# Kernel optimization log

Measured on AMD Instinct MI355X. Metric: run time of the kernel, lower is better.

## Reference

```python
import jax, jax.numpy as jnp
import numpy as np

N = 100000
E = 3200000
IN_DIM = 128
HD = 64
HEADS = 4
NEG_SLOPE = 0.2


def setup_inputs() -> dict:
    key = jax.random.key(0)
    ks = jax.random.split(key, 12)
    s = lambda fan_in: 1.0 / np.sqrt(fan_in)
    x = jax.random.normal(ks[0], (N, IN_DIM), dtype=jnp.float32)
    edge_index = jax.random.randint(ks[1], (2, E), 0, N, dtype=jnp.int64)
    W1 = jax.random.normal(ks[2], (IN_DIM, HEADS * HD), dtype=jnp.float32) * s(IN_DIM)
    a_src1 = jax.random.normal(ks[3], (HEADS, HD), dtype=jnp.float32) * s(HD)
    a_dst1 = jax.random.normal(ks[4], (HEADS, HD), dtype=jnp.float32) * s(HD)
    b1 = jnp.zeros((HEADS * HD,), dtype=jnp.float32)
    W2 = jax.random.normal(ks[5], (HEADS * HD, HD), dtype=jnp.float32) * s(HEADS * HD)
    a_src2 = jax.random.normal(ks[6], (1, HD), dtype=jnp.float32) * s(HD)
    a_dst2 = jax.random.normal(ks[7], (1, HD), dtype=jnp.float32) * s(HD)
    b2 = jnp.zeros((HD,), dtype=jnp.float32)
    lin_w = jax.random.normal(ks[8], (HD, 2), dtype=jnp.float32) * s(HD)
    lin_b = jnp.zeros((2,), dtype=jnp.float32)
    return {"x": x, "edge_index": edge_index, "W1": W1, "a_src1": a_src1,
            "a_dst1": a_dst1, "b1": b1, "W2": W2, "a_src2": a_src2,
            "a_dst2": a_dst2, "b2": b2, "lin_w": lin_w, "lin_b": lin_b}


def gat_conv(x, src, dst, W, a_src, a_dst, bias, heads, out_dim, concat):
    n = x.shape[0]
    h = (x @ W).reshape(n, heads, out_dim)                 # [N,H,D]
    alpha_s = jnp.einsum('nhd,hd->nh', h, a_src)           # [N,H]
    alpha_d = jnp.einsum('nhd,hd->nh', h, a_dst)           # [N,H]
    e = alpha_s[src] + alpha_d[dst]                        # [Etot,H]
    e = jnp.where(e > 0, e, NEG_SLOPE * e)                 # leaky relu
    m = jax.ops.segment_max(e, dst, num_segments=n)        # scatter-softmax (stable)
    m = jnp.where(jnp.isfinite(m), m, 0.0)
    e = jnp.exp(e - m[dst])
    denom = jax.ops.segment_sum(e, dst, num_segments=n)
    alpha = e / denom[dst]                                 # [Etot,H]
    out = jax.ops.segment_sum(h[src] * alpha[:, :, None], dst, num_segments=n)  # [N,H,D]
    out = out.reshape(n, heads * out_dim) if concat else out.mean(axis=1)
    return out + bias


def reference(x, edge_index, W1, a_src1, a_dst1, b1, W2, a_src2, a_dst2, b2, lin_w, lin_b):
    n = x.shape[0]
    loops = jnp.arange(n, dtype=edge_index.dtype)
    src = jnp.concatenate([edge_index[0], loops])          # add self-loops (PyG default)
    dst = jnp.concatenate([edge_index[1], loops])
    h = gat_conv(x, src, dst, W1, a_src1, a_dst1, b1, HEADS, HD, True)
    h = jax.nn.elu(h)
    h = gat_conv(h, src, dst, W2, a_src2, a_dst2, b2, 1, HD, True)
    h = jax.nn.elu(h)
    return h @ lin_w + lin_b                               # [N,2]
```

## Files before the change

### kernel.cpp

```cpp
#include <hip/hip_runtime.h>
#include <hip/hip_fp16.h>
#include <math.h>

#define NN 100000
#define EE 3200000
#define ETOT (EE + NN)
#define NEG_SLOPE 0.2f
#define DMAX 96
#define CHUNK 4096
#define NB0 ((ETOT + CHUNK - 1) / CHUNK)
#define RB 391
#define CAP 16384

typedef _Float16 half8 __attribute__((ext_vector_type(8)));
typedef _Float16 half4v __attribute__((ext_vector_type(4)));
typedef float floatx4 __attribute__((ext_vector_type(4)));

__device__ __forceinline__ float wsum64(float v) {
#pragma unroll
  for (int o = 32; o; o >>= 1) v += __shfl_xor(v, o);
  return v;
}
__device__ __forceinline__ float lrelu(float v) { return v > 0.f ? v : NEG_SLOPE * v; }
__device__ __forceinline__ float elu1(float v) { return v > 0.f ? v : expm1f(v); }

__global__ void k_init(int* __restrict__ ccur) {
  ccur[threadIdx.x] = threadIdx.x * CAP;
}

__global__ __launch_bounds__(256) void k_pass1(const int* __restrict__ ei,
                                               int* __restrict__ ccur,
                                               unsigned* __restrict__ ebuf,
                                               const float* __restrict__ W1,
                                               const float* __restrict__ W2,
                                               _Float16* __restrict__ W1t,
                                               _Float16* __restrict__ W2t) {
  int b = blockIdx.x;
  if (b >= NB0) {
    int idx = (b - NB0) * 256 + threadIdx.x;
    if (idx < 32768) {
      int n = idx >> 7, k = idx & 127;
      W1t[idx] = (_Float16)W1[k * 256 + n];
    } else {
      int j = idx - 32768;
      int n = j >> 8, k = j & 255;
      W2t[j] = (_Float16)W2[k * 64 + n];
    }
    return;
  }
  __shared__ unsigned vv[CHUNK];
  __shared__ unsigned short cbv[CHUNK];
  __shared__ int h[256];
  __shared__ int cur[256];
  int t = threadIdx.x;
  h[t] = 0;
  __syncthreads();
  int base = b * CHUNK;
  int lim = base + CHUNK; if (lim > ETOT) lim = ETOT;
  int cnt = lim - base;
  for (int i = t; i < cnt; i += 256) {
    int e = base + i;
    int s, d;
    if (e < EE) { s = ei[e]; d = ei[EE + e]; } else { s = e - EE; d = s; }
    unsigned cb = (unsigned)d / (unsigned)RB;
    unsigned dloc = (unsigned)d - cb * (unsigned)RB;
    vv[i] = (dloc << 17) | (unsigned)s;
    cbv[i] = (unsigned short)cb;
    atomicAdd(&h[cb], 1);
  }
  __syncthreads();
  if (h[t]) cur[t] = atomicAdd(&ccur[t], h[t]);
  __syncthreads();
  for (int i = t; i < cnt; i += 256) {
    int cb = cbv[i];
    int pos = atomicAdd(&cur[cb], 1);
    ebuf[pos] = vv[i];
  }
}

__global__ __launch_bounds__(256) void k_pass2(const unsigned* __restrict__ ebuf,
                                               const int* __restrict__ ccur,
                                               int* __restrict__ offs,
                                               int* __restrict__ degarr,
                                               int* __restrict__ csr) {
  __shared__ unsigned ed[CAP];
  __shared__ int hist[RB];
  __shared__ int cur[RB];
  int b = blockIdx.x, t = threadIdx.x;
  int d0 = b * RB;
  int rb = NN - d0; if (rb > RB) rb = RB;
  int w0 = b * CAP;
  int cnt = ccur[b] - w0;
  if (cnt > CAP) cnt = CAP;
  for (int j = t; j < rb; j += 256) hist[j] = 0;
  __syncthreads();
  for (int i = t; i < cnt; i += 256) {
    unsigned v = ebuf[w0 + i];
    ed[i] = v;
    atomicAdd(&hist[v >> 17], 1);
  }
  __syncthreads();
  if (t == 0) {
    int run = w0;
    for (int j = 0; j < rb; ++j) { cur[j] = run; run += hist[j]; }
  }
  __syncthreads();
  for (int j = t; j < rb; j += 256) {
    offs[d0 + j] = cur[j];
    degarr[d0 + j] = hist[j];
  }
  __syncthreads();
  for (int i = t; i < cnt; i += 256) {
    unsigned v = ed[i];
    int pos = atomicAdd(&cur[v >> 17], 1);
    csr[pos] = (int)(v & 0x1FFFFu);
  }
}

__global__ __launch_bounds__(256) void k_gemm1m(const float* __restrict__ x,
                                                const _Float16* __restrict__ W1t,
                                                const float* __restrict__ a_src,
                                                const float* __restrict__ a_dst,
                                                _Float16* __restrict__ h1h,
                                                float* __restrict__ as_out,
                                                float* __restrict__ ad_out) {
  __shared__ _Float16 As[64][136];
  __shared__ _Float16 Wt[128][136];
  const int bx = blockIdx.x & 1;
  const int by = blockIdx.x >> 1;
  const int tid = threadIdx.x;
  const int row0 = by * 64;
#pragma unroll
  for (int i = 0; i < 8; ++i) {
    int idx = i * 256 + tid;
    int r = idx >> 5;
    int c4 = (idx & 31) * 4;
    int gr = row0 + r;
    float4 f = make_float4(0.f, 0.f, 0.f, 0.f);
    if (gr < NN) f = *(const float4*)(x + (size_t)gr * 128 + c4);
    half4v h; h[0] = (_Float16)f.x; h[1] = (_Float16)f.y; h[2] = (_Float16)f.z; h[3] = (_Float16)f.w;
    *(half4v*)&As[r][c4] = h;
  }
#pragma unroll
  for (int i = 0; i < 8; ++i) {
    int idx = i * 256 + tid;
    int r = idx >> 4;
    int g = idx & 15;
    *(half8*)&Wt[r][g * 8] = *(const half8*)(W1t + (size_t)(bx * 128 + r) * 128 + g * 8);
  }
  __syncthreads();

  const int wid = tid >> 6, lane = tid & 63;
  const int m16 = lane & 15, quad = lane >> 4;
  floatx4 acc[8];
#pragma unroll
  for (int nt = 0; nt < 8; ++nt) acc[nt] = (floatx4){0.f, 0.f, 0.f, 0.f};
#pragma unroll
  for (int ks = 0; ks < 4; ++ks) {
    half8 av = *(half8*)&As[wid * 16 + m16][ks * 32 + quad * 8];
#pragma unroll
    for (int nt = 0; nt < 8; ++nt) {
      half8 bv = *(half8*)&Wt[nt * 16 + m16][ks * 32 + quad * 8];
      acc[nt] = __builtin_amdgcn_mfma_f32_16x16x32_f16(av, bv, acc[nt], 0, 0, 0);
    }
  }
  float asr[8], adr[8];
#pragma unroll
  for (int nt = 0; nt < 8; ++nt) {
    asr[nt] = a_src[bx * 128 + nt * 16 + m16];
    adr[nt] = a_dst[bx * 128 + nt * 16 + m16];
  }
#pragma unroll
  for (int r = 0; r < 4; ++r) {
    int gr = row0 + wid * 16 + quad * 4 + r;
    bool ok = gr < NN;
#pragma unroll
    for (int hp = 0; hp < 2; ++hp) {
      float ps = 0.f, pd = 0.f;
#pragma unroll
      for (int j = 0; j < 4; ++j) {
        ps = fmaf(acc[hp * 4 + j][r], asr[hp * 4 + j], ps);
        pd = fmaf(acc[hp * 4 + j][r], adr[hp * 4 + j], pd);
      }
#pragma unroll
      for (int o = 1; o < 16; o <<= 1) { ps += __shfl_xor(ps, o); pd += __shfl_xor(pd, o); }
      if (ok && m16 == 0) {
        as_out[gr * 4 + bx * 2 + hp] = ps;
        ad_out[gr * 4 + bx * 2 + hp] = pd;
      }
    }
    if (ok) {
#pragma unroll
      for (int nt = 0; nt < 8; ++nt)
        h1h[(size_t)gr * 256 + bx * 128 + nt * 16 + m16] = (_Float16)acc[nt][r];
    }
  }
}

__global__ __launch_bounds__(256) void k_gemm2m(const _Float16* __restrict__ h1e,
                                                const _Float16* __restrict__ W2t,
                                                const float* __restrict__ a_src,
                                                const float* __restrict__ a_dst,
                                                _Float16* __restrict__ h2h,
                                                float* __restrict__ as_out,
                                                float* __restrict__ ad_out) {
  __shared__ _Float16 As2[64][136];
  __shared__ _Float16 Wt2[64][264];
  const int by = blockIdx.x;
  const int tid = threadIdx.x;
  const int row0 = by * 64;
#pragma unroll
  for (int i = 0; i < 8; ++i) {
    int idx = i * 256 + tid;
    int r = idx >> 5;
    int g = idx & 31;
    *(half8*)&Wt2[r][g * 8] = *(const half8*)(W2t + (size_t)r * 256 + g * 8);
  }
  const int wid = tid >> 6, lane = tid & 63;
  const int m16 = lane & 15, quad = lane >> 4;
  floatx4 acc[4];
#pragma unroll
  for (int nt = 0; nt < 4; ++nt) acc[nt] = (floatx4){0.f, 0.f, 0.f, 0.f};

  for (int kc = 0; kc < 2; ++kc) {
#pragma unroll
    for (int i = 0; i < 4; ++i) {
      int idx = i * 256 + tid;
      int r = idx >> 4;
      int g = idx & 15;
      int gr = row0 + r;
      half8 v = {0, 0, 0, 0, 0, 0, 0, 0};
      if (gr < NN) v = *(const half8*)(h1e + (size_t)gr * 256 + kc * 128 + g * 8);
      *(half8*)&As2[r][g * 8] = v;
    }
    __syncthreads();
#pragma unroll
    for (int ks = 0; ks < 4; ++ks) {
      half8 av = *(half8*)&As2[wid * 16 + m16][ks * 32 + quad * 8];
#pragma unroll
      for (int nt = 0; nt < 4; ++nt) {
        half8 bv = *(half8*)&Wt2[nt * 16 + m16][kc * 128 + ks * 32 + quad * 8];
        acc[nt] = __builtin_amdgcn_mfma_f32_16x16x32_f16(av, bv, acc[nt], 0, 0, 0);
      }
    }
    __syncthreads();
  }
  float asr[4], adr[4];
#pragma unroll
  for (int nt = 0; nt < 4; ++nt) {
    asr[nt] = a_src[nt * 16 + m16];
    adr[nt] = a_dst[nt * 16 + m16];
  }
#pragma unroll
  for (int r = 0; r < 4; ++r) {
    float ps = 0.f, pd = 0.f;
#pragma unroll
    for (int nt = 0; nt < 4; ++nt) {
      ps = fmaf(acc[nt][r], asr[nt], ps);
      pd = fmaf(acc[nt][r], adr[nt], pd);
    }
#pragma unroll
    for (int o = 1; o < 16; o <<= 1) { ps += __shfl_xor(ps, o); pd += __shfl_xor(pd, o); }
    int gr = row0 + wid * 16 + quad * 4 + r;
    if (gr < NN) {
      if (m16 == 0) { as_out[gr] = ps; ad_out[gr] = pd; }
#pragma unroll
      for (int nt = 0; nt < 4; ++nt)
        h2h[(size_t)gr * 64 + nt * 16 + m16] = (_Float16)acc[nt][r];
    }
  }
}

__global__ __launch_bounds__(256) void k_attn1(const int* __restrict__ offs,
                                               const int* __restrict__ degarr,
                                               const int* __restrict__ csr_src,
                                               const float* __restrict__ a_s,
                                               const float* __restrict__ a_d,
                                               const _Float16* __restrict__ h1h,
                                               const float* __restrict__ b1,
                                               _Float16* __restrict__ h1e) {
  __shared__ float alpha[4][DMAX][4];
  __shared__ int sidx[4][DMAX];
  const int wid = threadIdx.x >> 6;
  const int n = blockIdx.x * 4 + wid;
  const int lane = threadIdx.x & 63;
  const int beg = offs[n], deg = degarr[n];
  const float4 ad = *(const float4*)(a_d + n * 4);
  float4 sm = make_float4(0.f, 0.f, 0.f, 0.f);
  for (int d = lane; d < deg; d += 64) {
    int s = csr_src[beg + d];
    float4 as = *(const float4*)(a_s + s * 4);
    float e0 = __expf(lrelu(as.x + ad.x));
    float e1 = __expf(lrelu(as.y + ad.y));
    float e2 = __expf(lrelu(as.z + ad.z));
    float e3 = __expf(lrelu(as.w + ad.w));
    sm.x += e0; sm.y += e1; sm.z += e2; sm.w += e3;
    if (d < DMAX) {
      sidx[wid][d] = s;
      *(float4*)&alpha[wid][d][0] = make_float4(e0, e1, e2, e3);
    }
  }
  sm.x = wsum64(sm.x); sm.y = wsum64(sm.y); sm.z = wsum64(sm.z); sm.w = wsum64(sm.w);
  const float4 inv4 = make_float4(1.f / sm.x, 1.f / sm.y, 1.f / sm.z, 1.f / sm.w);
  const int dlim = deg < DMAX ? deg : DMAX;
  for (int d = lane; d < dlim; d += 64) {
    float4 a = *(float4*)&alpha[wid][d][0];
    a.x *= inv4.x; a.y *= inv4.y; a.z *= inv4.z; a.w *= inv4.w;
    *(float4*)&alpha[wid][d][0] = a;
  }
  const int half = lane >> 5;
  const int sub = lane & 31;
  const int head = sub >> 3;
  const _Float16* __restrict__ hb = h1h + sub * 8;
  float accv[8];
#pragma unroll
  for (int j = 0; j < 8; ++j) accv[j] = 0.f;
  int d = 0;
  for (; d + 8 <= dlim; d += 8) {
    int ss[4]; float ww[4];
#pragma unroll
    for (int u = 0; u < 4; ++u) {
      int idx = d + 2 * u + half;
      ss[u] = sidx[wid][idx];
      ww[u] = alpha[wid][idx][head];
    }
    half8 rr[4];
#pragma unroll
    for (int u = 0; u < 4; ++u)
      rr[u] = *(const half8*)(hb + (size_t)ss[u] * 256);
#pragma unroll
    for (int u = 0; u < 4; ++u) {
#pragma unroll
      for (int j = 0; j < 8; ++j)
        accv[j] = fmaf((float)rr[u][j], ww[u], accv[j]);
    }
  }
  for (; d + 2 <= dlim; d += 2) {
    int idx = d + half;
    int s = sidx[wid][idx];
    float w = alpha[wid][idx][head];
    half8 r = *(const half8*)(hb + (size_t)s * 256);
#pragma unroll
    for (int j = 0; j < 8; ++j) accv[j] = fmaf((float)r[j], w, accv[j]);
  }
  if (d < dlim) {
    int s = sidx[wid][d];
    float w = half ? 0.f : alpha[wid][d][head];
    half8 r = *(const half8*)(hb + (size_t)s * 256);
#pragma unroll
    for (int j = 0; j < 8; ++j) accv[j] = fmaf((float)r[j], w, accv[j]);
  }
  if (deg > DMAX) {
    const float adh = head == 0 ? ad.x : head == 1 ? ad.y : head == 2 ? ad.z : ad.w;
    const float invh = head == 0 ? inv4.x : head == 1 ? inv4.y : head == 2 ? inv4.z : inv4.w;
    if (!half) {
      for (int dd = DMAX; dd < deg; ++dd) {
        int s = csr_src[beg + dd];
        float w = __expf(lrelu(a_s[s * 4 + head] + adh)) * invh;
        half8 r = *(const half8*)(hb + (size_t)s * 256);
#pragma unroll
        for (int j = 0; j < 8; ++j) accv[j] = fmaf((float)r[j], w, accv[j]);
      }
    }
  }
#pragma unroll
  for (int j = 0; j < 8; ++j) accv[j] += __shfl_xor(accv[j], 32);
  if (!half) {
    const int c = sub * 8;
    float4 b0 = *(const float4*)(b1 + c);
    float4 b1v = *(const float4*)(b1 + c + 4);
    half8 o;
    o[0] = (_Float16)elu1(accv[0] + b0.x);
    o[1] = (_Float16)elu1(accv[1] + b0.y);
    o[2] = (_Float16)elu1(accv[2] + b0.z);
    o[3] = (_Float16)elu1(accv[3] + b0.w);
    o[4] = (_Float16)elu1(accv[4] + b1v.x);
    o[5] = (_Float16)elu1(accv[5] + b1v.y);
    o[6] = (_Float16)elu1(accv[6] + b1v.z);
    o[7] = (_Float16)elu1(accv[7] + b1v.w);
    *(half8*)(h1e + (size_t)n * 256 + c) = o;
  }
}

__global__ __launch_bounds__(256) void k_attn2(const int* __restrict__ offs,
                                               const int* __restrict__ degarr,
                                               const int* __restrict__ csr_src,
                                               const float* __restrict__ a_s,
                                               const float* __restrict__ a_d,
                                               const _Float16* __restrict__ h2h,
                                               const float* __restrict__ b2,
                                               const float* __restrict__ lin_w,
                                               const float* __restrict__ lin_b,
                                               float* __restrict__ out) {
  __shared__ float alpha2[4][DMAX];
  __shared__ int sidx2[4][DMAX];
  const int wid = threadIdx.x >> 6;
  const int n = blockIdx.x * 4 + wid;
  const int lane = threadIdx.x & 63;
  const int beg = offs[n], deg = degarr[n];
  const float adn = a_d[n];
  float sm = 0.f;
  for (int d = lane; d < deg; d += 64) {
    int s = csr_src[beg + d];
    float e = __expf(lrelu(a_s[s] + adn));
    sm += e;
    if (d < DMAX) { sidx2[wid][d] = s; alpha2[wid][d] = e; }
  }
  sm = wsum64(sm);
  const float inv = 1.f / sm;
  const int dlim = deg < DMAX ? deg : DMAX;
  for (int d = lane; d < dlim; d += 64) alpha2[wid][d] *= inv;
  const int g = lane >> 4;
  const int sub = lane & 15;
  const _Float16* __restrict__ hb = h2h + sub * 4;
  float a0 = 0.f, a1 = 0.f, a2 = 0.f, a3 = 0.f;
  int d = 0;
  for (; d + 8 <= dlim; d += 8) {
    int i0 = d + g, i1 = d + 4 + g;
    int s0 = sidx2[wid][i0], s1 = sidx2[wid][i1];
    float w0 = alpha2[wid][i0], w1 = alpha2[wid][i1];
    half4v r0 = *(const half4v*)(hb + (size_t)s0 * 64);
    half4v r1 = *(const half4v*)(hb + (size_t)s1 * 64);
    a0 = fmaf((float)r0[0], w0, a0); a1 = fmaf((float)r0[1], w0, a1);
    a2 = fmaf((float)r0[2], w0, a2); a3 = fmaf((float)r0[3], w0, a3);
    a0 = fmaf((float)r1[0], w1, a0); a1 = fmaf((float)r1[1], w1, a1);
    a2 = fmaf((float)r1[2], w1, a2); a3 = fmaf((float)r1[3], w1, a3);
  }
  if (d + 4 <= dlim) {
    int i0 = d + g;
    int s0 = sidx2[wid][i0];
    float w0 = alpha2[wid][i0];
    half4v r0 = *(const half4v*)(hb + (size_t)s0 * 64);
    a0 = fmaf((float)r0[0], w0, a0); a1 = fmaf((float)r0[1], w0, a1);
    a2 = fmaf((float)r0[2], w0, a2); a3 = fmaf((float)r0[3], w0, a3);
    d += 4;
  }
  if (d < dlim) {
    int idx = d + g;
    bool v = idx < dlim;
    int s = sidx2[wid][v ? idx : d];
    float w = v ? alpha2[wid][idx] : 0.f;
    half4v r = *(const half4v*)(hb + (size_t)s * 64);
    a0 = fmaf((float)r[0], w, a0); a1 = fmaf((float)r[1], w, a1);
    a2 = fmaf((float)r[2], w, a2); a3 = fmaf((float)r[3], w, a3);
  }
  if (deg > DMAX && g == 0) {
    for (int dd = DMAX; dd < deg; ++dd) {
      int s = csr_src[beg + dd];
      float w = __expf(lrelu(a_s[s] + adn)) * inv;
      half4v r = *(const half4v*)(hb + (size_t)s * 64);
      a0 = fmaf((float)r[0], w, a0); a1 = fmaf((float)r[1], w, a1);
      a2 = fmaf((float)r[2], w, a2); a3 = fmaf((float)r[3], w, a3);
    }
  }
  a0 += __shfl_xor(a0, 16); a1 += __shfl_xor(a1, 16);
  a2 += __shfl_xor(a2, 16); a3 += __shfl_xor(a3, 16);
  a0 += __shfl_xor(a0, 32); a1 += __shfl_xor(a1, 32);
  a2 += __shfl_xor(a2, 32); a3 += __shfl_xor(a3, 32);
  const int c = sub * 4;
  float4 bb = *(const float4*)(b2 + c);
  float o0 = elu1(a0 + bb.x);
  float o1 = elu1(a1 + bb.y);
  float o2 = elu1(a2 + bb.z);
  float o3 = elu1(a3 + bb.w);
  float4 lw0 = *(const float4*)(lin_w + c * 2);
  float4 lw1 = *(const float4*)(lin_w + c * 2 + 4);
  float p0 = o0 * lw0.x + o1 * lw0.z + o2 * lw1.x + o3 * lw1.z;
  float p1 = o0 * lw0.y + o1 * lw0.w + o2 * lw1.y + o3 * lw1.w;
  p0 = wsum64(p0) * 0.25f;
  p1 = wsum64(p1) * 0.25f;
  if (lane == 0) {
    out[n * 2 + 0] = p0 + lin_b[0];
    out[n * 2 + 1] = p1 + lin_b[1];
  }
}

extern "C" void kernel_launch(void* const* d_in, const int* in_sizes, int n_in,
                              void* d_out, int out_size, void* d_ws, size_t ws_size,
                              hipStream_t stream) {
  const float* x      = (const float*)d_in[0];
  const int*   ei     = (const int*)d_in[1];
  const float* W1     = (const float*)d_in[2];
  const float* a_src1 = (const float*)d_in[3];
  const float* a_dst1 = (const float*)d_in[4];
  const float* b1     = (const float*)d_in[5];
  const float* W2     = (const float*)d_in[6];
  const float* a_src2 = (const float*)d_in[7];
  const float* a_dst2 = (const float*)d_in[8];
  const float* b2     = (const float*)d_in[9];
  const float* lin_w  = (const float*)d_in[10];
  const float* lin_b  = (const float*)d_in[11];
  float* outp = (float*)d_out;

  char* w = (char*)d_ws;
  _Float16* h1h = (_Float16*)(w + 0);
  _Float16* h1e = (_Float16*)(w + 51200000);
  _Float16* h2h = (_Float16*)(w + 102400000);
  _Float16* W1t = (_Float16*)(w + 115200000);
  _Float16* W2t = (_Float16*)(w + 115265536);
  float*  as1 = (float*)(w + 115298304);
  float*  ad1 = (float*)(w + 116898304);
  float*  as2 = (float*)(w + 118498304);
  float*  ad2 = (float*)(w + 118898304);
  int*    offs = (int*)(w + 119298304);
  int*    degarr = (int*)(w + 119698304);
  int*    ccur = (int*)(w + 120098304);
  unsigned* ebuf = (unsigned*)(w + 120099328);
  int*    csr = (int*)(w + 136876544);

  k_init<<<1, 256, 0, stream>>>(ccur);
  k_pass1<<<NB0 + 192, 256, 0, stream>>>(ei, ccur, ebuf, W1, W2, W1t, W2t);
  k_pass2<<<256, 256, 0, stream>>>(ebuf, ccur, offs, degarr, csr);

  k_gemm1m<<<2 * 1563, 256, 0, stream>>>(x, W1t, a_src1, a_dst1, h1h, as1, ad1);
  k_attn1<<<NN / 4, 256, 0, stream>>>(offs, degarr, csr, as1, ad1, h1h, b1, h1e);

  k_gemm2m<<<1563, 256, 0, stream>>>(h1e, W2t, a_src2, a_dst2, h2h, as2, ad2);
  k_attn2<<<NN / 4, 256, 0, stream>>>(offs, degarr, csr, as2, ad2, h2h, b2, lin_w, lin_b, outp);
}
```

Before: 574.3 us.

## Aggregate raw features before layer-1 projection and fuse both GEMMs

Layer 1 is reordered so the attention-weighted aggregation runs on the 128-wide fp16 input per head, and the W1 projection is applied afterward. The attention logits come from x·(W1·a), which is precomputed inside the prep kernel. A new kernel fuses the per-head W1 GEMM, bias, ELU and the W2 GEMM with the layer-2 logits. This halves per-edge gather width and drops the h1h/h1e round trips, at the cost of writing and reading a 4×128 per-node aggregate buffer and doing more FMAs per gathered row.

Result: slower. 594.2 us (+3.5%).

```diff
diff --git a/kernel.cpp b/kernel.cpp
--- a/kernel.cpp
+++ b/kernel.cpp
@@ -11,9 +11,11 @@
 #define NB0 ((ETOT + CHUNK - 1) / CHUNK)
 #define RB 391
 #define CAP 16384
+#define PREPB 391
 
 typedef _Float16 half8 __attribute__((ext_vector_type(8)));
 typedef _Float16 half4v __attribute__((ext_vector_type(4)));
+typedef _Float16 half2v __attribute__((ext_vector_type(2)));
 typedef float floatx4 __attribute__((ext_vector_type(4)));
 
 __device__ __forceinline__ float wsum64(float v) {
@@ -34,10 +36,48 @@
                                                const float* __restrict__ W1,
                                                const float* __restrict__ W2,
                                                _Float16* __restrict__ W1t,
-                                               _Float16* __restrict__ W2t) {
-  int b = blockIdx.x;
-  if (b >= NB0) {
-    int idx = (b - NB0) * 256 + threadIdx.x;
+                                               _Float16* __restrict__ W2t,
+                                               const float* __restrict__ x,
+                                               const float* __restrict__ a_src1,
+                                               const float* __restrict__ a_dst1,
+                                               _Float16* __restrict__ xh,
+                                               float* __restrict__ as1,
+                                               float* __restrict__ ad1) {
+  __shared__ __align__(16) char smem[26624];
+  const int b = blockIdx.x;
+  const int t = threadIdx.x;
+  if (b < NB0) {
+    unsigned* vv = (unsigned*)smem;
+    unsigned short* cbv = (unsigned short*)(smem + 16384);
+    int* h = (int*)(smem + 24576);
+    int* cur = (int*)(smem + 25600);
+    h[t] = 0;
+    __syncthreads();
+    int base = b * CHUNK;
+    int lim = base + CHUNK; if (lim > ETOT) lim = ETOT;
+    int cnt = lim - base;
+    for (int i = t; i < cnt; i += 256) {
+      int e = base + i;
+      int s, d;
+      if (e < EE) { s = ei[e]; d = ei[EE + e]; } else { s = e - EE; d = s; }
+      unsigned cb = (unsigned)d / (unsigned)RB;
+      unsigned dloc = (unsigned)d - cb * (unsigned)RB;
+      vv[i] = (dloc << 17) | (unsigned)s;
+      cbv[i] = (unsigned short)cb;
+      atomicAdd(&h[cb], 1);
+    }
+    __syncthreads();
+    if (h[t]) cur[t] = atomicAdd(&ccur[t], h[t]);
+    __syncthreads();
+    for (int i = t; i < cnt; i += 256) {
+      int cb = cbv[i];
+      int pos = atomicAdd(&cur[cb], 1);
+      ebuf[pos] = vv[i];
+    }
+    return;
+  }
+  if (b < NB0 + 192) {
+    int idx = (b - NB0) * 256 + t;
     if (idx < 32768) {
       int n = idx >> 7, k = idx & 127;
       W1t[idx] = (_Float16)W1[k * 256 + n];
@@ -48,33 +88,39 @@
     }
     return;
   }
-  __shared__ unsigned vv[CHUNK];
-  __shared__ unsigned short cbv[CHUNK];
-  __shared__ int h[256];
-  __shared__ int cur[256];
-  int t = threadIdx.x;
-  h[t] = 0;
+  float* vs = (float*)smem;
+  float* vd = vs + 512;
+  for (int i = t; i < 512; i += 256) {
+    int h = i >> 7, k = i & 127;
+    const float* wrow = W1 + (size_t)k * 256 + h * 64;
+    float ss = 0.f, dd = 0.f;
+#pragma unroll 8
+    for (int d2 = 0; d2 < 64; ++d2) {
+      float wv = wrow[d2];
+      ss = fmaf(wv, a_src1[h * 64 + d2], ss);
+      dd = fmaf(wv, a_dst1[h * 64 + d2], dd);
+    }
+    vs[i] = ss; vd[i] = dd;
+  }
   __syncthreads();
-  int base = b * CHUNK;
-  int lim = base + CHUNK; if (lim > ETOT) lim = ETOT;
-  int cnt = lim - base;
-  for (int i = t; i < cnt; i += 256) {
-    int e = base + i;
-    int s, d;
-    if (e < EE) { s = ei[e]; d = ei[EE + e]; } else { s = e - EE; d = s; }
-    unsigned cb = (unsigned)d / (unsigned)RB;
-    unsigned dloc = (unsigned)d - cb * (unsigned)RB;
-    vv[i] = (dloc << 17) | (unsigned)s;
-    cbv[i] = (unsigned short)cb;
-    atomicAdd(&h[cb], 1);
-  }
-  __syncthreads();
-  if (h[t]) cur[t] = atomicAdd(&ccur[t], h[t]);
-  __syncthreads();
-  for (int i = t; i < cnt; i += 256) {
-    int cb = cbv[i];
-    int pos = atomicAdd(&cur[cb], 1);
-    ebuf[pos] = vv[i];
+  const int lane = t & 63;
+  const int gw = (b - NB0 - 192) * 4 + (t >> 6);
+  for (int n = gw; n < NN; n += 4 * PREPB) {
+    float2 xv = *(const float2*)(x + (size_t)n * 128 + lane * 2);
+    half2v hx; hx[0] = (_Float16)xv.x; hx[1] = (_Float16)xv.y;
+    *(half2v*)(xh + (size_t)n * 128 + lane * 2) = hx;
+    float p[8];
+#pragma unroll
+    for (int h = 0; h < 4; ++h) {
+      p[h]     = xv.x * vs[h * 128 + lane * 2] + xv.y * vs[h * 128 + lane * 2 + 1];
+      p[4 + h] = xv.x * vd[h * 128 + lane * 2] + xv.y * vd[h * 128 + lane * 2 + 1];
+    }
+#pragma unroll
+    for (int j = 0; j < 8; ++j) p[j] = wsum64(p[j]);
+    if (lane == 0) {
+      *(float4*)(as1 + n * 4) = make_float4(p[0], p[1], p[2], p[3]);
+      *(float4*)(ad1 + n * 4) = make_float4(p[4], p[5], p[6], p[7]);
+    }
   }
 }
 
@@ -117,169 +163,14 @@
   }
 }
 
-__global__ __launch_bounds__(256) void k_gemm1m(const float* __restrict__ x,
-                                                const _Float16* __restrict__ W1t,
-                                                const float* __restrict__ a_src,
-                                                const float* __restrict__ a_dst,
-                                                _Float16* __restrict__ h1h,
-                                                float* __restrict__ as_out,
-                                                float* __restrict__ ad_out) {
-  __shared__ _Float16 As[64][136];
-  __shared__ _Float16 Wt[128][136];
-  const int bx = blockIdx.x & 1;
-  const int by = blockIdx.x >> 1;
-  const int tid = threadIdx.x;
-  const int row0 = by * 64;
-#pragma unroll
-  for (int i = 0; i < 8; ++i) {
-    int idx = i * 256 + tid;
-    int r = idx >> 5;
-    int c4 = (idx & 31) * 4;
-    int gr = row0 + r;
-    float4 f = make_float4(0.f, 0.f, 0.f, 0.f);
-    if (gr < NN) f = *(const float4*)(x + (size_t)gr * 128 + c4);
-    half4v h; h[0] = (_Float16)f.x; h[1] = (_Float16)f.y; h[2] = (_Float16)f.z; h[3] = (_Float16)f.w;
-    *(half4v*)&As[r][c4] = h;
-  }
-#pragma unroll
-  for (int i = 0; i < 8; ++i) {
-    int idx = i * 256 + tid;
-    int r = idx >> 4;
-    int g = idx & 15;
-    *(half8*)&Wt[r][g * 8] = *(const half8*)(W1t + (size_t)(bx * 128 + r) * 128 + g * 8);
-  }
-  __syncthreads();
-
-  const int wid = tid >> 6, lane = tid & 63;
-  const int m16 = lane & 15, quad = lane >> 4;
-  floatx4 acc[8];
-#pragma unroll
-  for (int nt = 0; nt < 8; ++nt) acc[nt] = (floatx4){0.f, 0.f, 0.f, 0.f};
-#pragma unroll
-  for (int ks = 0; ks < 4; ++ks) {
-    half8 av = *(half8*)&As[wid * 16 + m16][ks * 32 + quad * 8];
-#pragma unroll
-    for (int nt = 0; nt < 8; ++nt) {
-      half8 bv = *(half8*)&Wt[nt * 16 + m16][ks * 32 + quad * 8];
-      acc[nt] = __builtin_amdgcn_mfma_f32_16x16x32_f16(av, bv, acc[nt], 0, 0, 0);
-    }
-  }
-  float asr[8], adr[8];
-#pragma unroll
-  for (int nt = 0; nt < 8; ++nt) {
-    asr[nt] = a_src[bx * 128 + nt * 16 + m16];
-    adr[nt] = a_dst[bx * 128 + nt * 16 + m16];
-  }
-#pragma unroll
-  for (int r = 0; r < 4; ++r) {
-    int gr = row0 + wid * 16 + quad * 4 + r;
-    bool ok = gr < NN;
-#pragma unroll
-    for (int hp = 0; hp < 2; ++hp) {
-      float ps = 0.f, pd = 0.f;
-#pragma unroll
-      for (int j = 0; j < 4; ++j) {
-        ps = fmaf(acc[hp * 4 + j][r], asr[hp * 4 + j], ps);
-        pd = fmaf(acc[hp * 4 + j][r], adr[hp * 4 + j], pd);
-      }
-#pragma unroll
-      for (int o = 1; o < 16; o <<= 1) { ps += __shfl_xor(ps, o); pd += __shfl_xor(pd, o); }
-      if (ok && m16 == 0) {
-        as_out[gr * 4 + bx * 2 + hp] = ps;
-        ad_out[gr * 4 + bx * 2 + hp] = pd;
-      }
-    }
-    if (ok) {
-#pragma unroll
-      for (int nt = 0; nt < 8; ++nt)
-        h1h[(size_t)gr * 256 + bx * 128 + nt * 16 + m16] = (_Float16)acc[nt][r];
-    }
-  }
-}
-
-__global__ __launch_bounds__(256) void k_gemm2m(const _Float16* __restrict__ h1e,
-                                                const _Float16* __restrict__ W2t,
-                                                const float* __restrict__ a_src,
-                                                const float* __restrict__ a_dst,
-                                                _Float16* __restrict__ h2h,
-                                                float* __restrict__ as_out,
-                                                float* __restrict__ ad_out) {
-  __shared__ _Float16 As2[64][136];
-  __shared__ _Float16 Wt2[64][264];
-  const int by = blockIdx.x;
-  const int tid = threadIdx.x;
-  const int row0 = by * 64;
-#pragma unroll
-  for (int i = 0; i < 8; ++i) {
-    int idx = i * 256 + tid;
-    int r = idx >> 5;
-    int g = idx & 31;
-    *(half8*)&Wt2[r][g * 8] = *(const half8*)(W2t + (size_t)r * 256 + g * 8);
-  }
-  const int wid = tid >> 6, lane = tid & 63;
-  const int m16 = lane & 15, quad = lane >> 4;
-  floatx4 acc[4];
-#pragma unroll
-  for (int nt = 0; nt < 4; ++nt) acc[nt] = (floatx4){0.f, 0.f, 0.f, 0.f};
-
-  for (int kc = 0; kc < 2; ++kc) {
-#pragma unroll
-    for (int i = 0; i < 4; ++i) {
-      int idx = i * 256 + tid;
-      int r = idx >> 4;
-      int g = idx & 15;
-      int gr = row0 + r;
-      half8 v = {0, 0, 0, 0, 0, 0, 0, 0};
-      if (gr < NN) v = *(const half8*)(h1e + (size_t)gr * 256 + kc * 128 + g * 8);
-      *(half8*)&As2[r][g * 8] = v;
-    }
-    __syncthreads();
-#pragma unroll
-    for (int ks = 0; ks < 4; ++ks) {
-      half8 av = *(half8*)&As2[wid * 16 + m16][ks * 32 + quad * 8];
-#pragma unroll
-      for (int nt = 0; nt < 4; ++nt) {
-        half8 bv = *(half8*)&Wt2[nt * 16 + m16][kc * 128 + ks * 32 + quad * 8];
-        acc[nt] = __builtin_amdgcn_mfma_f32_16x16x32_f16(av, bv, acc[nt], 0, 0, 0);
-      }
-    }
-    __syncthreads();
-  }
-  float asr[4], adr[4];
-#pragma unroll
-  for (int nt = 0; nt < 4; ++nt) {
-    asr[nt] = a_src[nt * 16 + m16];
-    adr[nt] = a_dst[nt * 16 + m16];
-  }
-#pragma unroll
-  for (int r = 0; r < 4; ++r) {
-    float ps = 0.f, pd = 0.f;
-#pragma unroll
-    for (int nt = 0; nt < 4; ++nt) {
-      ps = fmaf(acc[nt][r], asr[nt], ps);
-      pd = fmaf(acc[nt][r], adr[nt], pd);
-    }
-#pragma unroll
-    for (int o = 1; o < 16; o <<= 1) { ps += __shfl_xor(ps, o); pd += __shfl_xor(pd, o); }
-    int gr = row0 + wid * 16 + quad * 4 + r;
-    if (gr < NN) {
-      if (m16 == 0) { as_out[gr] = ps; ad_out[gr] = pd; }
-#pragma unroll
-      for (int nt = 0; nt < 4; ++nt)
-        h2h[(size_t)gr * 64 + nt * 16 + m16] = (_Float16)acc[nt][r];
-    }
-  }
-}
-
-__global__ __launch_bounds__(256) void k_attn1(const int* __restrict__ offs,
-                                               const int* __restrict__ degarr,
-                                               const int* __restrict__ csr_src,
-                                               const float* __restrict__ a_s,
-                                               const float* __restrict__ a_d,
-                                               const _Float16* __restrict__ h1h,
-                                               const float* __restrict__ b1,
-                                               _Float16* __restrict__ h1e) {
-  __shared__ float alpha[4][DMAX][4];
+__global__ __launch_bounds__(256) void k_agg1(const int* __restrict__ offs,
+                                              const int* __restrict__ degarr,
+                                              const int* __restrict__ csr_src,
+                                              const float* __restrict__ a_s,
+                                              const float* __restrict__ a_d,
+                                              const _Float16* __restrict__ xh,
+                                              _Float16* __restrict__ agg) {
+  __shared__ __align__(16) float alp[4][DMAX][4];
   __shared__ int sidx[4][DMAX];
   const int wid = threadIdx.x >> 6;
   const int n = blockIdx.x * 4 + wid;
@@ -297,88 +188,191 @@
     sm.x += e0; sm.y += e1; sm.z += e2; sm.w += e3;
     if (d < DMAX) {
       sidx[wid][d] = s;
-      *(float4*)&alpha[wid][d][0] = make_float4(e0, e1, e2, e3);
+      *(float4*)&alp[wid][d][0] = make_float4(e0, e1, e2, e3);
     }
   }
   sm.x = wsum64(sm.x); sm.y = wsum64(sm.y); sm.z = wsum64(sm.z); sm.w = wsum64(sm.w);
   const float4 inv4 = make_float4(1.f / sm.x, 1.f / sm.y, 1.f / sm.z, 1.f / sm.w);
   const int dlim = deg < DMAX ? deg : DMAX;
   for (int d = lane; d < dlim; d += 64) {
-    float4 a = *(float4*)&alpha[wid][d][0];
+    float4 a = *(float4*)&alp[wid][d][0];
     a.x *= inv4.x; a.y *= inv4.y; a.z *= inv4.z; a.w *= inv4.w;
-    *(float4*)&alpha[wid][d][0] = a;
-  }
-  const int half = lane >> 5;
-  const int sub = lane & 31;
-  const int head = sub >> 3;
-  const _Float16* __restrict__ hb = h1h + sub * 8;
-  float accv[8];
-#pragma unroll
-  for (int j = 0; j < 8; ++j) accv[j] = 0.f;
+    *(float4*)&alp[wid][d][0] = a;
+  }
+  const int g = lane >> 4;
+  const int sub = lane & 15;
+  const _Float16* __restrict__ hb = xh + sub * 8;
+  float acc[4][8];
+#pragma unroll
+  for (int h = 0; h < 4; ++h)
+#pragma unroll
+    for (int j = 0; j < 8; ++j) acc[h][j] = 0.f;
   int d = 0;
   for (; d + 8 <= dlim; d += 8) {
-    int ss[4]; float ww[4];
-#pragma unroll
-    for (int u = 0; u < 4; ++u) {
-      int idx = d + 2 * u + half;
-      ss[u] = sidx[wid][idx];
-      ww[u] = alpha[wid][idx][head];
-    }
-    half8 rr[4];
-#pragma unroll
-    for (int u = 0; u < 4; ++u)
-      rr[u] = *(const half8*)(hb + (size_t)ss[u] * 256);
-#pragma unroll
-    for (int u = 0; u < 4; ++u) {
-#pragma unroll
-      for (int j = 0; j < 8; ++j)
-        accv[j] = fmaf((float)rr[u][j], ww[u], accv[j]);
-    }
-  }
-  for (; d + 2 <= dlim; d += 2) {
-    int idx = d + half;
-    int s = sidx[wid][idx];
-    float w = alpha[wid][idx][head];
-    half8 r = *(const half8*)(hb + (size_t)s * 256);
-#pragma unroll
-    for (int j = 0; j < 8; ++j) accv[j] = fmaf((float)r[j], w, accv[j]);
+    int i0 = d + g, i1 = d + 4 + g;
+    int s0 = sidx[wid][i0], s1 = sidx[wid][i1];
+    float4 w0 = *(float4*)&alp[wid][i0][0];
+    float4 w1 = *(float4*)&alp[wid][i1][0];
+    half8 r0 = *(const half8*)(hb + (size_t)s0 * 128);
+    half8 r1 = *(const half8*)(hb + (size_t)s1 * 128);
+#pragma unroll
+    for (int j = 0; j < 8; ++j) {
+      float f0 = (float)r0[j], f1 = (float)r1[j];
+      acc[0][j] = fmaf(f0, w0.x, acc[0][j]);
+      acc[1][j] = fmaf(f0, w0.y, acc[1][j]);
+      acc[2][j] = fmaf(f0, w0.z, acc[2][j]);
+      acc[3][j] = fmaf(f0, w0.w, acc[3][j]);
+      acc[0][j] = fmaf(f1, w1.x, acc[0][j]);
+      acc[1][j] = fmaf(f1, w1.y, acc[1][j]);
+      acc[2][j] = fmaf(f1, w1.z, acc[2][j]);
+      acc[3][j] = fmaf(f1, w1.w, acc[3][j]);
+    }
+  }
+  if (d + 4 <= dlim) {
+    int i0 = d + g;
+    int s0 = sidx[wid][i0];
+    float4 w0 = *(float4*)&alp[wid][i0][0];
+    half8 r0 = *(const half8*)(hb + (size_t)s0 * 128);
+#pragma unroll
+    for (int j = 0; j < 8; ++j) {
+      float f0 = (float)r0[j];
+      acc[0][j] = fmaf(f0, w0.x, acc[0][j]);
+      acc[1][j] = fmaf(f0, w0.y, acc[1][j]);
+      acc[2][j] = fmaf(f0, w0.z, acc[2][j]);
+      acc[3][j] = fmaf(f0, w0.w, acc[3][j]);
+    }
+    d += 4;
   }
   if (d < dlim) {
-    int s = sidx[wid][d];
-    float w = half ? 0.f : alpha[wid][d][head];
-    half8 r = *(const half8*)(hb + (size_t)s * 256);
-#pragma unroll
-    for (int j = 0; j < 8; ++j) accv[j] = fmaf((float)r[j], w, accv[j]);
+    int idx = d + g;
+    bool v = idx < dlim;
+    int s = sidx[wid][v ? idx : d];
+    float4 w0 = *(float4*)&alp[wid][v ? idx : d][0];
+    if (!v) { w0.x = 0.f; w0.y = 0.f; w0.z = 0.f; w0.w = 0.f; }
+    half8 r0 = *(const half8*)(hb + (size_t)s * 128);
+#pragma unroll
+    for (int j = 0; j < 8; ++j) {
+      float f0 = (float)r0[j];
+      acc[0][j] = fmaf(f0, w0.x, acc[0][j]);
+      acc[1][j] = fmaf(f0, w0.y, acc[1][j]);
+      acc[2][j] = fmaf(f0, w0.z, acc[2][j]);
+      acc[3][j] = fmaf(f0, w0.w, acc[3][j]);
+    }
   }
   if (deg > DMAX) {
-    const float adh = head == 0 ? ad.x : head == 1 ? ad.y : head == 2 ? ad.z : ad.w;
-    const float invh = head == 0 ? inv4.x : head == 1 ? inv4.y : head == 2 ? inv4.z : inv4.w;
-    if (!half) {
-      for (int dd = DMAX; dd < deg; ++dd) {
-        int s = csr_src[beg + dd];
-        float w = __expf(lrelu(a_s[s * 4 + head] + adh)) * invh;
-        half8 r = *(const half8*)(hb + (size_t)s * 256);
-#pragma unroll
-        for (int j = 0; j < 8; ++j) accv[j] = fmaf((float)r[j], w, accv[j]);
+    for (int dd = DMAX + g; dd < deg; dd += 4) {
+      int s = csr_src[beg + dd];
+      float4 as = *(const float4*)(a_s + s * 4);
+      float w0x = __expf(lrelu(as.x + ad.x)) * inv4.x;
+      float w0y = __expf(lrelu(as.y + ad.y)) * inv4.y;
+      float w0z = __expf(lrelu(as.z + ad.z)) * inv4.z;
+      float w0w = __expf(lrelu(as.w + ad.w)) * inv4.w;
+      half8 r0 = *(const half8*)(hb + (size_t)s * 128);
+#pragma unroll
+      for (int j = 0; j < 8; ++j) {
+        float f0 = (float)r0[j];
+        acc[0][j] = fmaf(f0, w0x, acc[0][j]);
+        acc[1][j] = fmaf(f0, w0y, acc[1][j]);
+        acc[2][j] = fmaf(f0, w0z, acc[2][j]);
+        acc[3][j] = fmaf(f0, w0w, acc[3][j]);
       }
     }
   }
 #pragma unroll
-  for (int j = 0; j < 8; ++j) accv[j] += __shfl_xor(accv[j], 32);
-  if (!half) {
-    const int c = sub * 8;
-    float4 b0 = *(const float4*)(b1 + c);
-    float4 b1v = *(const float4*)(b1 + c + 4);
-    half8 o;
-    o[0] = (_Float16)elu1(accv[0] + b0.x);
-    o[1] = (_Float16)elu1(accv[1] + b0.y);
-    o[2] = (_Float16)elu1(accv[2] + b0.z);
-    o[3] = (_Float16)elu1(accv[3] + b0.w);
-    o[4] = (_Float16)elu1(accv[4] + b1v.x);
-    o[5] = (_Float16)elu1(accv[5] + b1v.y);
-    o[6] = (_Float16)elu1(accv[6] + b1v.z);
-    o[7] = (_Float16)elu1(accv[7] + b1v.w);
-    *(half8*)(h1e + (size_t)n * 256 + c) = o;
+  for (int h = 0; h < 4; ++h)
+#pragma unroll
+    for (int j = 0; j < 8; ++j) {
+      acc[h][j] += __shfl_xor(acc[h][j], 16);
+      acc[h][j] += __shfl_xor(acc[h][j], 32);
+    }
+  if (g == 0) {
+#pragma unroll
+    for (int h = 0; h < 4; ++h) {
+      half8 o;
+#pragma unroll
+      for (int j = 0; j < 8; ++j) o[j] = (_Float16)acc[h][j];
+      *(half8*)(agg + ((size_t)n * 4 + h) * 128 + sub * 8) = o;
+    }
+  }
+}
+
+__global__ __launch_bounds__(256) void k_gemmAgg2(const _Float16* __restrict__ agg,
+                                                  const _Float16* __restrict__ W1t,
+                                                  const _Float16* __restrict__ W2t,
+                                                  const float* __restrict__ b1,
+                                                  const float* __restrict__ a_src2,
+                                                  const float* __restrict__ a_dst2,
+                                                  _Float16* __restrict__ h2h,
+                                                  float* __restrict__ as_out,
+                                                  float* __restrict__ ad_out) {
+  __shared__ _Float16 h1eT[64][264];
+  const int tid = threadIdx.x;
+  const int row0 = blockIdx.x * 64;
+  const int wid = tid >> 6, lane = tid & 63;
+  const int m16 = lane & 15, quad = lane >> 4;
+  floatx4 acc1[4][4];
+#pragma unroll
+  for (int h = 0; h < 4; ++h)
+#pragma unroll
+    for (int nt = 0; nt < 4; ++nt) acc1[h][nt] = (floatx4){0.f, 0.f, 0.f, 0.f};
+  const size_t arow = (size_t)(row0 + wid * 16 + m16) * 512;
+#pragma unroll
+  for (int h = 0; h < 4; ++h) {
+#pragma unroll
+    for (int ks = 0; ks < 4; ++ks) {
+      half8 av = *(const half8*)(agg + arow + h * 128 + ks * 32 + quad * 8);
+#pragma unroll
+      for (int nt = 0; nt < 4; ++nt) {
+        half8 bv = *(const half8*)(W1t + (size_t)(h * 64 + nt * 16 + m16) * 128 + ks * 32 + quad * 8);
+        acc1[h][nt] = __builtin_amdgcn_mfma_f32_16x16x32_f16(av, bv, acc1[h][nt], 0, 0, 0);
+      }
+    }
+  }
+#pragma unroll
+  for (int h = 0; h < 4; ++h)
+#pragma unroll
+    for (int nt = 0; nt < 4; ++nt) {
+      float bb = b1[h * 64 + nt * 16 + m16];
+#pragma unroll
+      for (int r = 0; r < 4; ++r)
+        h1eT[wid * 16 + quad * 4 + r][h * 64 + nt * 16 + m16] = (_Float16)elu1(acc1[h][nt][r] + bb);
+    }
+  __syncthreads();
+  floatx4 acc2[4];
+#pragma unroll
+  for (int nt = 0; nt < 4; ++nt) acc2[nt] = (floatx4){0.f, 0.f, 0.f, 0.f};
+#pragma unroll
+  for (int ks = 0; ks < 8; ++ks) {
+    half8 av = *(const half8*)&h1eT[wid * 16 + m16][ks * 32 + quad * 8];
+#pragma unroll
+    for (int nt = 0; nt < 4; ++nt) {
+      half8 bv = *(const half8*)(W2t + (size_t)(nt * 16 + m16) * 256 + ks * 32 + quad * 8);
+      acc2[nt] = __builtin_amdgcn_mfma_f32_16x16x32_f16(av, bv, acc2[nt], 0, 0, 0);
+    }
+  }
+  float asr[4], adr[4];
+#pragma unroll
+  for (int nt = 0; nt < 4; ++nt) {
+    asr[nt] = a_src2[nt * 16 + m16];
+    adr[nt] = a_dst2[nt * 16 + m16];
+  }
+#pragma unroll
+  for (int r = 0; r < 4; ++r) {
+    float ps = 0.f, pd = 0.f;
+#pragma unroll
+    for (int nt = 0; nt < 4; ++nt) {
+      ps = fmaf(acc2[nt][r], asr[nt], ps);
+      pd = fmaf(acc2[nt][r], adr[nt], pd);
+    }
+#pragma unroll
+    for (int o = 1; o < 16; o <<= 1) { ps += __shfl_xor(ps, o); pd += __shfl_xor(pd, o); }
+    int gr = row0 + wid * 16 + quad * 4 + r;
+    if (gr < NN) {
+      if (m16 == 0) { as_out[gr] = ps; ad_out[gr] = pd; }
+#pragma unroll
+      for (int nt = 0; nt < 4; ++nt)
+        h2h[(size_t)gr * 64 + nt * 16 + m16] = (_Float16)acc2[nt][r];
+    }
   }
 }
 
@@ -493,28 +487,28 @@
   float* outp = (float*)d_out;
 
   char* w = (char*)d_ws;
-  _Float16* h1h = (_Float16*)(w + 0);
-  _Float16* h1e = (_Float16*)(w + 51200000);
-  _Float16* h2h = (_Float16*)(w + 102400000);
-  _Float16* W1t = (_Float16*)(w + 115200000);
-  _Float16* W2t = (_Float16*)(w + 115265536);
-  float*  as1 = (float*)(w + 115298304);
-  float*  ad1 = (float*)(w + 116898304);
-  float*  as2 = (float*)(w + 118498304);
-  float*  ad2 = (float*)(w + 118898304);
-  int*    offs = (int*)(w + 119298304);
-  int*    degarr = (int*)(w + 119698304);
-  int*    ccur = (int*)(w + 120098304);
-  unsigned* ebuf = (unsigned*)(w + 120099328);
-  int*    csr = (int*)(w + 136876544);
+  _Float16* agg  = (_Float16*)(w + 0);
+  unsigned* ebuf = (unsigned*)(w + 33554432);
+  _Float16* xh   = (_Float16*)(w + 102432768);
+  _Float16* h2h  = (_Float16*)(w + 102432768);
+  int*    csr    = (int*)(w + 128032768);
+  _Float16* W1t  = (_Float16*)(w + 144809984);
+  _Float16* W2t  = (_Float16*)(w + 144875520);
+  float*  as1    = (float*)(w + 144908288);
+  float*  ad1    = (float*)(w + 146508288);
+  float*  as2    = (float*)(w + 148108288);
+  float*  ad2    = (float*)(w + 148508288);
+  int*    offs   = (int*)(w + 148908288);
+  int*    degarr = (int*)(w + 149308288);
+  int*    ccur   = (int*)(w + 149708288);
 
   k_init<<<1, 256, 0, stream>>>(ccur);
-  k_pass1<<<NB0 + 192, 256, 0, stream>>>(ei, ccur, ebuf, W1, W2, W1t, W2t);
+  k_pass1<<<NB0 + 192 + PREPB, 256, 0, stream>>>(ei, ccur, ebuf, W1, W2, W1t, W2t,
+                                                 x, a_src1, a_dst1, xh, as1, ad1);
   k_pass2<<<256, 256, 0, stream>>>(ebuf, ccur, offs, degarr, csr);
 
-  k_gemm1m<<<2 * 1563, 256, 0, stream>>>(x, W1t, a_src1, a_dst1, h1h, as1, ad1);
-  k_attn1<<<NN / 4, 256, 0, stream>>>(offs, degarr, csr, as1, ad1, h1h, b1, h1e);
-
-  k_gemm2m<<<1563, 256, 0, stream>>>(h1e, W2t, a_src2, a_dst2, h2h, as2, ad2);
+  k_agg1<<<NN / 4, 256, 0, stream>>>(offs, degarr, csr, as1, ad1, xh, agg);
+  k_gemmAgg2<<<1563, 256, 0, stream>>>(agg, W1t, W2t, b1, a_src2, a_dst2, h2h, as2, ad2);
+
   k_attn2<<<NN / 4, 256, 0, stream>>>(offs, degarr, csr, as2, ad2, h2h, b2, lin_w, lin_b, outp);
 }
```
